# Optimization experiments

Measured on AMD Instinct MI355X. Metric: run time of the kernel, lower is better.

## Reference

```python
import jax, jax.numpy as jnp
import numpy as np

EPS = 1e-5
TAU = 2.0
HEADS = 8
SCALE = 0.125


def _bn(y, g, b, m, v):
    # y: [TB, C, N]; per-channel eval-mode batchnorm
    inv = jax.lax.rsqrt(v + EPS)
    return (y - m[:, None]) * (g * inv)[:, None] + b[:, None]


def _lif(x_seq, vth):
    # spikingjelly MultiStepLIFNode: v += (x - v)/tau, spike = H(v - vth), hard reset v*(1-s)
    def step(mem, xt):
        mem = mem + (xt - mem) / TAU
        s = (mem >= vth).astype(xt.dtype)
        mem = mem * (1.0 - s)
        return mem, s
    _, spikes = jax.lax.scan(step, jnp.zeros_like(x_seq[0]), x_seq)
    return spikes


def setup_inputs() -> dict:
    key = jax.random.key(0)
    ks = jax.random.split(key, 8)
    T, B, C, H, W = 4, 16, 256, 32, 32
    d = {
        'x': jax.random.normal(ks[0], (T, B, C, H, W), jnp.float32),
        'res_attn': jnp.zeros((1,), jnp.float32),
    }
    for i, p in enumerate(['q', 'k', 'v']):
        d[p + '_w'] = jax.random.normal(ks[1 + i], (C, C), jnp.float32) * 0.02
        d[p + '_gamma'] = jnp.ones((C,), jnp.float32)
        d[p + '_beta'] = jnp.zeros((C,), jnp.float32)
        d[p + '_mean'] = jnp.zeros((C,), jnp.float32)
        d[p + '_var'] = jnp.ones((C,), jnp.float32)
    d['p_w'] = jax.random.normal(ks[4], (C, C), jnp.float32) * 0.02
    d['p_b'] = jnp.zeros((C,), jnp.float32)
    d['p_gamma'] = jnp.ones((C,), jnp.float32)
    d['p_beta'] = jnp.zeros((C,), jnp.float32)
    d['p_mean'] = jnp.zeros((C,), jnp.float32)
    d['p_var'] = jnp.ones((C,), jnp.float32)
    return d


def reference(x, res_attn, q_w, q_gamma, q_beta, q_mean, q_var,
              k_w, k_gamma, k_beta, k_mean, k_var,
              v_w, v_gamma, v_beta, v_mean, v_var,
              p_w, p_b, p_gamma, p_beta, p_mean, p_var):
    T, B, C, H, W = x.shape
    N = H * W
    d = C // HEADS
    x2 = x.reshape(T * B, C, N)

    def branch(w, g, b, m, v):
        y = _bn(jnp.einsum('oc,bcn->bon', w, x2), g, b, m, v).reshape(T, B, C, N)
        s = _lif(y, 1.0)  # [T,B,C,N]
        # -> [T,B,heads,N,d]
        return s.transpose(0, 1, 3, 2).reshape(T, B, N, HEADS, d).transpose(0, 1, 3, 2, 4)

    q = branch(q_w, q_gamma, q_beta, q_mean, q_var)
    k = branch(k_w, k_gamma, k_beta, k_mean, k_var)
    v = branch(v_w, v_gamma, v_beta, v_mean, v_var)

    kv = jnp.einsum('tbhnd,tbhne->tbhde', k, v)      # [T,B,h,d,d]
    attn = jnp.einsum('tbhnd,tbhde->tbhne', q, kv) * SCALE  # [T,B,h,N,d]
    xa = attn.transpose(0, 1, 2, 4, 3).reshape(T, B, C, N)
    xa = _lif(xa, 0.5)

    y = _bn(jnp.einsum('oc,bcn->bon', p_w, xa.reshape(T * B, C, N)) + p_b[:, None],
            p_gamma, p_beta, p_mean, p_var)
    out = _lif(y.reshape(T, B, C, H, W), 1.0)
    return (out, v)
```

## Files before the change

### kernel.cpp

```cpp
#include <hip/hip_runtime.h>
#include <stdint.h>

typedef unsigned int u32;
typedef unsigned short ushort_t;

#define T_ 4
#define B_ 16
#define C_ 256
#define N_ 1024
#define CN (C_ * N_)
#define M_ELEMS (64 * C_ * N_)

#define OFF_S    0ull
#define OFF_YP   0ull
#define OFF_XC   67108864ull
#define OFF_SC   67108864ull
#define OFF_KV   134217728ull
#define OFF_BNS  136314880ull
#define OFF_WC   136331264ull
#define OFF_WPC  137510912ull

typedef __attribute__((ext_vector_type(8))) short bf16x8;
typedef __attribute__((ext_vector_type(4))) float f32x4;

__device__ __forceinline__ ushort_t f2bf(float f) {
  u32 u = __float_as_uint(f);
  u32 r = (u + 0x7FFFu + ((u >> 16) & 1u)) >> 16;
  return (ushort_t)r;
}
__device__ __forceinline__ float bf2f(ushort_t h) { return __uint_as_float((u32)h << 16); }

__device__ __forceinline__ void async_copy16(const void* g, void* l) {
  __builtin_amdgcn_global_load_lds(
      (const __attribute__((address_space(1))) u32*)g,
      (__attribute__((address_space(3))) u32*)l, 16, 0, 0);
}

__global__ void bn_prep(const float* __restrict__ qg, const float* __restrict__ qb2, const float* __restrict__ qm, const float* __restrict__ qv,
                        const float* __restrict__ kg, const float* __restrict__ kb, const float* __restrict__ km, const float* __restrict__ kvv,
                        const float* __restrict__ vg, const float* __restrict__ vb, const float* __restrict__ vm, const float* __restrict__ vv,
                        const float* __restrict__ pbias,
                        const float* __restrict__ pg, const float* __restrict__ pbt, const float* __restrict__ pm, const float* __restrict__ pv,
                        float* __restrict__ bns) {
  int i = threadIdx.x;
  int br = i >> 8, c = i & 255;
  const float *g, *bt, *m, *v;
  float bias = 0.f;
  if (br == 0)      { g = qg; bt = qb2; m = qm; v = qv; }
  else if (br == 1) { g = kg; bt = kb;  m = km; v = kvv; }
  else if (br == 2) { g = vg; bt = vb;  m = vm; v = vv; }
  else              { g = pg; bt = pbt; m = pm; v = pv; bias = pbias[c]; }
  float sc = g[c] / sqrtf(v[c] + 1e-5f);
  float sh = bt[c] + (bias - m[c]) * sc;
  float rcp = (sc != 0.f) ? (1.f / sc) : 0.f;
  *(float4*)&bns[4 * i] = make_float4(sc, sh, rcp, 0.f);
}

__global__ __launch_bounds__(256) void convert_w(const float* __restrict__ qw, const float* __restrict__ kw,
                                                 const float* __restrict__ vw, const float* __restrict__ pw,
                                                 ushort_t* __restrict__ Wc, ushort_t* __restrict__ Wpc) {
  int id = blockIdx.x * 256 + threadIdx.x;
  int br = id >> 16, o = (id >> 8) & 255, c = id & 255;
  const float* w = (br == 0) ? qw : (br == 1) ? kw : (br == 2) ? vw : pw;
  float f = w[o * 256 + c];
  ushort_t hi = f2bf(f);
  ushort_t lo = f2bf(f - bf2f(hi));
  if (br < 3) {
    ushort_t* d = Wc + (size_t)br * 196608 + (size_t)o * 768 + c;
    d[0] = hi; d[256] = lo; d[512] = hi;
  } else {
    ushort_t* d = Wpc + (size_t)o * 512 + c;
    d[0] = hi; d[256] = lo;
  }
}

__global__ __launch_bounds__(256) void convert_x(const float* __restrict__ x, ushort_t* __restrict__ Xc) {
  __shared__ ushort_t hi[32][260];
  __shared__ ushort_t lo[32][260];
  int bid = blockIdx.x;
  int nc = bid & 3, kb = (bid >> 2) & 7, tb = bid >> 5;
  int t = threadIdx.x;
  int n0 = nc * 256;
  const float* xb = x + (size_t)tb * CN + (size_t)(kb * 32) * N_ + n0;
#pragma unroll
  for (int p = 0; p < 8; ++p) {
    int k = p * 4 + (t >> 6);
    int n4 = (t & 63) * 4;
    float4 v = *(const float4*)&xb[(size_t)k * N_ + n4];
    ushort_t h0 = f2bf(v.x), h1 = f2bf(v.y), h2 = f2bf(v.z), h3 = f2bf(v.w);
    short4 hv = make_short4((short)h0, (short)h1, (short)h2, (short)h3);
    short4 lv = make_short4((short)f2bf(v.x - bf2f(h0)), (short)f2bf(v.y - bf2f(h1)),
                            (short)f2bf(v.z - bf2f(h2)), (short)f2bf(v.w - bf2f(h3)));
    *(short4*)&hi[k][n4] = hv;
    *(short4*)&lo[k][n4] = lv;
  }
  __syncthreads();
  ushort_t* Hs = Xc + ((size_t)(tb * 16 + kb) * 1024 + n0) * 32;
  ushort_t* Ls = Xc + ((size_t)(tb * 16 + 8 + kb) * 1024 + n0) * 32;
  int kq = t & 3;
#pragma unroll
  for (int q = 0; q < 4; ++q) {
    int n = q * 64 + (t >> 2);
    u32 a0 = (u32)hi[kq * 8 + 0][n] | ((u32)hi[kq * 8 + 1][n] << 16);
    u32 a1 = (u32)hi[kq * 8 + 2][n] | ((u32)hi[kq * 8 + 3][n] << 16);
    u32 a2 = (u32)hi[kq * 8 + 4][n] | ((u32)hi[kq * 8 + 5][n] << 16);
    u32 a3 = (u32)hi[kq * 8 + 6][n] | ((u32)hi[kq * 8 + 7][n] << 16);
    *(uint4*)(Hs + (size_t)n * 32 + kq * 8) = make_uint4(a0, a1, a2, a3);
    u32 b0 = (u32)lo[kq * 8 + 0][n] | ((u32)lo[kq * 8 + 1][n] << 16);
    u32 b1 = (u32)lo[kq * 8 + 2][n] | ((u32)lo[kq * 8 + 3][n] << 16);
    u32 b2 = (u32)lo[kq * 8 + 4][n] | ((u32)lo[kq * 8 + 5][n] << 16);
    u32 b3 = (u32)lo[kq * 8 + 6][n] | ((u32)lo[kq * 8 + 7][n] << 16);
    *(uint4*)(Ls + (size_t)n * 32 + kq * 8) = make_uint4(b0, b1, b2, b3);
  }
}

__global__ __launch_bounds__(256, 3) void gemm_qkv_lif(
    const ushort_t* __restrict__ Wc, const ushort_t* __restrict__ Xc,
    const float* __restrict__ bns, uint8_t* __restrict__ S) {
  __shared__ ushort_t Al[128 * 32];
  __shared__ ushort_t Bl[128 * 32];
  const int nt = blockIdx.x, mt = blockIdx.y, b = blockIdx.z;
  const int br = mt >> 1, rh = mt & 1;
  const ushort_t* Ab = Wc + (size_t)br * 196608 + (size_t)(rh * 128) * 768;
  const int tid = threadIdx.x;
  const int lane = tid & 63;
  const int quad = lane >> 4, r = lane & 15;
  const int w = tid >> 6;
  const int moff = (w & 1) * 64, noff = (w >> 1) * 64;
  const int c0 = tid, c1 = tid + 256;

  f32x4 acc[16];
#pragma unroll
  for (int f = 0; f < 16; ++f) acc[f] = (f32x4){0.f, 0.f, 0.f, 0.f};

  for (int t = 0; t < 4; ++t) {
    const ushort_t* Xtb = Xc + (size_t)(t * 16 + b) * 16 * 32768 + (size_t)(nt * 128) * 32;
    for (int kb = 0; kb < 24; ++kb) {
      const int kbm = (kb < 8) ? kb : kb - 8;
      const ushort_t* Acol = Ab + kb * 32;
      async_copy16(Acol + (size_t)(c0 >> 2) * 768 + (c0 & 3) * 8, &Al[c0 * 8]);
      async_copy16(Acol + (size_t)(c1 >> 2) * 768 + (c1 & 3) * 8, &Al[c1 * 8]);
      const ushort_t* Bb = Xtb + (size_t)kbm * 32768;
      async_copy16(Bb + c0 * 8, &Bl[c0 * 8]);
      async_copy16(Bb + c1 * 8, &Bl[c1 * 8]);
      __syncthreads();
      bf16x8 a0 = *(const bf16x8*)&Al[(moff + 0 * 16 + r) * 32 + quad * 8];
      bf16x8 a1 = *(const bf16x8*)&Al[(moff + 1 * 16 + r) * 32 + quad * 8];
      bf16x8 a2 = *(const bf16x8*)&Al[(moff + 2 * 16 + r) * 32 + quad * 8];
      bf16x8 a3 = *(const bf16x8*)&Al[(moff + 3 * 16 + r) * 32 + quad * 8];
      bf16x8 b0 = *(const bf16x8*)&Bl[(noff + 0 * 16 + r) * 32 + quad * 8];
      bf16x8 b1 = *(const bf16x8*)&Bl[(noff + 1 * 16 + r) * 32 + quad * 8];
      bf16x8 b2 = *(const bf16x8*)&Bl[(noff + 2 * 16 + r) * 32 + quad * 8];
      bf16x8 b3 = *(const bf16x8*)&Bl[(noff + 3 * 16 + r) * 32 + quad * 8];
      acc[0]  = __builtin_amdgcn_mfma_f32_16x16x32_bf16(a0, b0, acc[0],  0, 0, 0);
      acc[1]  = __builtin_amdgcn_mfma_f32_16x16x32_bf16(a0, b1, acc[1],  0, 0, 0);
      acc[2]  = __builtin_amdgcn_mfma_f32_16x16x32_bf16(a0, b2, acc[2],  0, 0, 0);
      acc[3]  = __builtin_amdgcn_mfma_f32_16x16x32_bf16(a0, b3, acc[3],  0, 0, 0);
      acc[4]  = __builtin_amdgcn_mfma_f32_16x16x32_bf16(a1, b0, acc[4],  0, 0, 0);
      acc[5]  = __builtin_amdgcn_mfma_f32_16x16x32_bf16(a1, b1, acc[5],  0, 0, 0);
      acc[6]  = __builtin_amdgcn_mfma_f32_16x16x32_bf16(a1, b2, acc[6],  0, 0, 0);
      acc[7]  = __builtin_amdgcn_mfma_f32_16x16x32_bf16(a1, b3, acc[7],  0, 0, 0);
      acc[8]  = __builtin_amdgcn_mfma_f32_16x16x32_bf16(a2, b0, acc[8],  0, 0, 0);
      acc[9]  = __builtin_amdgcn_mfma_f32_16x16x32_bf16(a2, b1, acc[9],  0, 0, 0);
      acc[10] = __builtin_amdgcn_mfma_f32_16x16x32_bf16(a2, b2, acc[10], 0, 0, 0);
      acc[11] = __builtin_amdgcn_mfma_f32_16x16x32_bf16(a2, b3, acc[11], 0, 0, 0);
      acc[12] = __builtin_amdgcn_mfma_f32_16x16x32_bf16(a3, b0, acc[12], 0, 0, 0);
      acc[13] = __builtin_amdgcn_mfma_f32_16x16x32_bf16(a3, b1, acc[13], 0, 0, 0);
      acc[14] = __builtin_amdgcn_mfma_f32_16x16x32_bf16(a3, b2, acc[14], 0, 0, 0);
      acc[15] = __builtin_amdgcn_mfma_f32_16x16x32_bf16(a3, b3, acc[15], 0, 0, 0);
      __syncthreads();
    }
    uint8_t* Sb = S + (size_t)br * M_ELEMS + (size_t)(t * 16 + b) * CN;
#pragma unroll
    for (int i = 0; i < 4; ++i) {
#pragma unroll
      for (int rg = 0; rg < 4; ++rg) {
        int c = rh * 128 + moff + i * 16 + quad * 4 + rg;
        float4 bn = *(const float4*)&bns[4 * (br * 256 + c)];
        float hsc = 0.5f * bn.x;
        float hsh = 0.5f * bn.y;
        float rcp = bn.z;
        uint8_t* row = Sb + (size_t)c * N_ + nt * 128 + noff + r;
#pragma unroll
        for (int j = 0; j < 4; ++j) {
          float m = acc[i * 4 + j][rg] * hsc + hsh;
          uint8_t s = (m >= 1.0f) ? 1 : 0;
          row[j * 16] = s;
          acc[i * 4 + j][rg] = s ? 0.f : m * rcp;
        }
      }
    }
  }
}

__global__ __launch_bounds__(256) void transpose_v(const uint8_t* __restrict__ SV, float* __restrict__ vout) {
  size_t o4 = ((size_t)blockIdx.x * 256 + threadIdx.x) * 4;
  int dd = (int)(o4 & 31);
  int n = (int)((o4 >> 5) & 1023);
  int h = (int)((o4 >> 15) & 7);
  int tb = (int)(o4 >> 18);
  const uint8_t* src = SV + (size_t)tb * CN + (size_t)(h * 32 + dd) * N_ + n;
  *(float4*)(vout + o4) = make_float4((float)src[0], (float)src[(size_t)N_],
                                      (float)src[2 * (size_t)N_], (float)src[3 * (size_t)N_]);
}

__global__ __launch_bounds__(256) void kv_gram(const uint8_t* __restrict__ SK,
                                               const uint8_t* __restrict__ SV,
                                               float* __restrict__ KV) {
  __shared__ uint8_t Ks[32 * 132];
  __shared__ uint8_t Vs[32 * 132];
  const int tb = blockIdx.x >> 3, h = blockIdx.x & 7;
  const uint8_t* K = SK + (size_t)tb * CN + (size_t)h * 32 * N_;
  const uint8_t* V = SV + (size_t)tb * CN + (size_t)h * 32 * N_;
  const int tid = threadIdx.x;
  const int dd = tid >> 3, e0 = (tid & 7) * 4;
  const int lr = tid >> 3, lc = (tid & 7) * 16;
  float a0 = 0.f, a1 = 0.f, a2 = 0.f, a3 = 0.f;
  for (int n0 = 0; n0 < N_; n0 += 128) {
    uint4 kk4 = *(const uint4*)(K + (size_t)lr * N_ + n0 + lc);
    uint4 vv4 = *(const uint4*)(V + (size_t)lr * N_ + n0 + lc);
    unsigned* Kw = (unsigned*)(Ks + lr * 132 + lc);
    unsigned* Vw = (unsigned*)(Vs + lr * 132 + lc);
    Kw[0] = kk4.x; Kw[1] = kk4.y; Kw[2] = kk4.z; Kw[3] = kk4.w;
    Vw[0] = vv4.x; Vw[1] = vv4.y; Vw[2] = vv4.z; Vw[3] = vv4.w;
    __syncthreads();
    for (int n = 0; n < 128; ++n) {
      float kf = (float)Ks[dd * 132 + n];
      a0 += kf * (float)Vs[(e0 + 0) * 132 + n];
      a1 += kf * (float)Vs[(e0 + 1) * 132 + n];
      a2 += kf * (float)Vs[(e0 + 2) * 132 + n];
      a3 += kf * (float)Vs[(e0 + 3) * 132 + n];
    }
    __syncthreads();
  }
  float* o = KV + (size_t)(tb * 8 + h) * 1024 + dd * 32 + e0;
  o[0] = a0; o[1] = a1; o[2] = a2; o[3] = a3;
}

__global__ __launch_bounds__(256) void attn_lif(const uint8_t* __restrict__ SQ,
                                                const float* __restrict__ KV,
                                                ushort_t* __restrict__ Sc) {
  __shared__ float kvs[1024];
  const int bid = blockIdx.x;
  const int nb = bid & 15, h = (bid >> 4) & 7, b = bid >> 7;
  const int n0 = nb * 64;
  const int tid = threadIdx.x;
  const int nl = tid & 63, eg = tid >> 6;
  float mem[8];
#pragma unroll
  for (int j = 0; j < 8; ++j) mem[j] = 0.f;
  for (int t = 0; t < 4; ++t) {
    const float* kvp = KV + (size_t)((t * B_ + b) * 8 + h) * 1024;
    *(float4*)&kvs[tid * 4] = *(const float4*)&kvp[tid * 4];
    __syncthreads();
    const uint8_t* q = SQ + (size_t)(t * B_ + b) * CN + (size_t)h * 32 * N_ + n0 + nl;
    float val[8];
#pragma unroll
    for (int j = 0; j < 8; ++j) val[j] = 0.f;
#pragma unroll 4
    for (int dd = 0; dd < 32; ++dd) {
      float qv = (float)q[(size_t)dd * N_];
#pragma unroll
      for (int j = 0; j < 8; ++j) val[j] += qv * kvs[dd * 32 + eg * 8 + j];
    }
    ushort_t pk[8];
#pragma unroll
    for (int j = 0; j < 8; ++j) {
      float a = val[j] * 0.125f;
      mem[j] += (a - mem[j]) * 0.5f;
      int s = (mem[j] >= 0.5f);
      pk[j] = s ? (ushort_t)0x3F80 : (ushort_t)0;
      if (s) mem[j] = 0.f;
    }
    uint4 o;
    o.x = (u32)pk[0] | ((u32)pk[1] << 16);
    o.y = (u32)pk[2] | ((u32)pk[3] << 16);
    o.z = (u32)pk[4] | ((u32)pk[5] << 16);
    o.w = (u32)pk[6] | ((u32)pk[7] << 16);
    *(uint4*)(Sc + ((size_t)((t * B_ + b) * 8 + h) * 1024 + n0 + nl) * 32 + eg * 8) = o;
    __syncthreads();
  }
}

__global__ __launch_bounds__(256, 3) void gemm_p_mfma(
    const ushort_t* __restrict__ Wpc, const ushort_t* __restrict__ Sc,
    const float* __restrict__ bns, float* __restrict__ YP) {
  __shared__ ushort_t Al[128 * 32];
  __shared__ ushort_t Bl[128 * 32];
  const int nt = blockIdx.x, mt = blockIdx.y, tb = blockIdx.z;
  const ushort_t* Ab = Wpc + (size_t)(mt * 128) * 512;
  const int tid = threadIdx.x;
  const int lane = tid & 63;
  const int quad = lane >> 4, r = lane & 15;
  const int w = tid >> 6;
  const int moff = (w & 1) * 64, noff = (w >> 1) * 64;
  const int c0 = tid, c1 = tid + 256;
  f32x4 acc[16];
#pragma unroll
  for (int f = 0; f < 16; ++f) acc[f] = (f32x4){0.f, 0.f, 0.f, 0.f};
  const ushort_t* Stb = Sc + (size_t)tb * 8 * 32768 + (size_t)(nt * 128) * 32;
  for (int kb = 0; kb < 16; ++kb) {
    const int kbm = (kb < 8) ? kb : kb - 8;
    const ushort_t* Acol = Ab + kb * 32;
    async_copy16(Acol + (size_t)(c0 >> 2) * 512 + (c0 & 3) * 8, &Al[c0 * 8]);
    async_copy16(Acol + (size_t)(c1 >> 2) * 512 + (c1 & 3) * 8, &Al[c1 * 8]);
    const ushort_t* Bb = Stb + (size_t)kbm * 32768;
    async_copy16(Bb + c0 * 8, &Bl[c0 * 8]);
    async_copy16(Bb + c1 * 8, &Bl[c1 * 8]);
    __syncthreads();
    bf16x8 a0 = *(const bf16x8*)&Al[(moff + 0 * 16 + r) * 32 + quad * 8];
    bf16x8 a1 = *(const bf16x8*)&Al[(moff + 1 * 16 + r) * 32 + quad * 8];
    bf16x8 a2 = *(const bf16x8*)&Al[(moff + 2 * 16 + r) * 32 + quad * 8];
    bf16x8 a3 = *(const bf16x8*)&Al[(moff + 3 * 16 + r) * 32 + quad * 8];
    bf16x8 b0 = *(const bf16x8*)&Bl[(noff + 0 * 16 + r) * 32 + quad * 8];
    bf16x8 b1 = *(const bf16x8*)&Bl[(noff + 1 * 16 + r) * 32 + quad * 8];
    bf16x8 b2 = *(const bf16x8*)&Bl[(noff + 2 * 16 + r) * 32 + quad * 8];
    bf16x8 b3 = *(const bf16x8*)&Bl[(noff + 3 * 16 + r) * 32 + quad * 8];
    acc[0]  = __builtin_amdgcn_mfma_f32_16x16x32_bf16(a0, b0, acc[0],  0, 0, 0);
    acc[1]  = __builtin_amdgcn_mfma_f32_16x16x32_bf16(a0, b1, acc[1],  0, 0, 0);
    acc[2]  = __builtin_amdgcn_mfma_f32_16x16x32_bf16(a0, b2, acc[2],  0, 0, 0);
    acc[3]  = __builtin_amdgcn_mfma_f32_16x16x32_bf16(a0, b3, acc[3],  0, 0, 0);
    acc[4]  = __builtin_amdgcn_mfma_f32_16x16x32_bf16(a1, b0, acc[4],  0, 0, 0);
    acc[5]  = __builtin_amdgcn_mfma_f32_16x16x32_bf16(a1, b1, acc[5],  0, 0, 0);
    acc[6]  = __builtin_amdgcn_mfma_f32_16x16x32_bf16(a1, b2, acc[6],  0, 0, 0);
    acc[7]  = __builtin_amdgcn_mfma_f32_16x16x32_bf16(a1, b3, acc[7],  0, 0, 0);
    acc[8]  = __builtin_amdgcn_mfma_f32_16x16x32_bf16(a2, b0, acc[8],  0, 0, 0);
    acc[9]  = __builtin_amdgcn_mfma_f32_16x16x32_bf16(a2, b1, acc[9],  0, 0, 0);
    acc[10] = __builtin_amdgcn_mfma_f32_16x16x32_bf16(a2, b2, acc[10], 0, 0, 0);
    acc[11] = __builtin_amdgcn_mfma_f32_16x16x32_bf16(a2, b3, acc[11], 0, 0, 0);
    acc[12] = __builtin_amdgcn_mfma_f32_16x16x32_bf16(a3, b0, acc[12], 0, 0, 0);
    acc[13] = __builtin_amdgcn_mfma_f32_16x16x32_bf16(a3, b1, acc[13], 0, 0, 0);
    acc[14] = __builtin_amdgcn_mfma_f32_16x16x32_bf16(a3, b2, acc[14], 0, 0, 0);
    acc[15] = __builtin_amdgcn_mfma_f32_16x16x32_bf16(a3, b3, acc[15], 0, 0, 0);
    __syncthreads();
  }
  float* Yb = YP + (size_t)tb * CN;
#pragma unroll
  for (int i = 0; i < 4; ++i) {
#pragma unroll
    for (int rg = 0; rg < 4; ++rg) {
      int c = mt * 128 + moff + i * 16 + quad * 4 + rg;
      float4 bn = *(const float4*)&bns[4 * (768 + c)];
      float sc = bn.x;
      float sh = bn.y;
      float* row = Yb + (size_t)c * N_ + nt * 128 + noff + r;
#pragma unroll
      for (int j = 0; j < 4; ++j) row[j * 16] = acc[i * 4 + j][rg] * sc + sh;
    }
  }
}

__global__ __launch_bounds__(256) void lif_out(const float* __restrict__ YP, float* __restrict__ out) {
  size_t e4 = ((size_t)blockIdx.x * 256 + threadIdx.x) * 4;
  float m0 = 0.f, m1 = 0.f, m2 = 0.f, m3 = 0.f;
#pragma unroll
  for (int t = 0; t < 4; ++t) {
    float4 y = *(const float4*)(YP + (size_t)t * (B_ * CN) + e4);
    m0 += (y.x - m0) * 0.5f;
    m1 += (y.y - m1) * 0.5f;
    m2 += (y.z - m2) * 0.5f;
    m3 += (y.w - m3) * 0.5f;
    float s0 = (m0 >= 1.0f) ? 1.f : 0.f;
    float s1 = (m1 >= 1.0f) ? 1.f : 0.f;
    float s2 = (m2 >= 1.0f) ? 1.f : 0.f;
    float s3 = (m3 >= 1.0f) ? 1.f : 0.f;
    *(float4*)(out + (size_t)t * (B_ * CN) + e4) = make_float4(s0, s1, s2, s3);
    m0 *= (1.f - s0);
    m1 *= (1.f - s1);
    m2 *= (1.f - s2);
    m3 *= (1.f - s3);
  }
}

extern "C" void kernel_launch(void* const* d_in, const int* in_sizes, int n_in,
                              void* d_out, int out_size, void* d_ws, size_t ws_size,
                              hipStream_t stream) {
  const float* x   = (const float*)d_in[0];
  const float* qw  = (const float*)d_in[2];
  const float* qg  = (const float*)d_in[3];
  const float* qb  = (const float*)d_in[4];
  const float* qm  = (const float*)d_in[5];
  const float* qv  = (const float*)d_in[6];
  const float* kw  = (const float*)d_in[7];
  const float* kg  = (const float*)d_in[8];
  const float* kb  = (const float*)d_in[9];
  const float* km  = (const float*)d_in[10];
  const float* kvv = (const float*)d_in[11];
  const float* vw  = (const float*)d_in[12];
  const float* vg  = (const float*)d_in[13];
  const float* vb  = (const float*)d_in[14];
  const float* vm  = (const float*)d_in[15];
  const float* vv  = (const float*)d_in[16];
  const float* pw  = (const float*)d_in[17];
  const float* pb  = (const float*)d_in[18];
  const float* pg  = (const float*)d_in[19];
  const float* pbt = (const float*)d_in[20];
  const float* pm  = (const float*)d_in[21];
  const float* pv  = (const float*)d_in[22];

  float* out = (float*)d_out;
  float* vout = out + M_ELEMS;

  uint8_t* ws = (uint8_t*)d_ws;
  uint8_t* S   = ws + OFF_S;
  float* YP    = (float*)(ws + OFF_YP);
  ushort_t* Xc = (ushort_t*)(ws + OFF_XC);
  ushort_t* Sc = (ushort_t*)(ws + OFF_SC);
  float* KV    = (float*)(ws + OFF_KV);
  float* BNS   = (float*)(ws + OFF_BNS);
  ushort_t* Wc  = (ushort_t*)(ws + OFF_WC);
  ushort_t* Wpc = (ushort_t*)(ws + OFF_WPC);

  bn_prep<<<dim3(1), dim3(1024), 0, stream>>>(qg, qb, qm, qv, kg, kb, km, kvv,
                                              vg, vb, vm, vv, pb, pg, pbt, pm, pv, BNS);
  convert_w<<<dim3(1024), dim3(256), 0, stream>>>(qw, kw, vw, pw, Wc, Wpc);
  convert_x<<<dim3(2048), dim3(256), 0, stream>>>(x, Xc);
  gemm_qkv_lif<<<dim3(8, 6, 16), dim3(256), 0, stream>>>(Wc, Xc, BNS, S);
  transpose_v<<<dim3(16384), dim3(256), 0, stream>>>(S + 2ull * M_ELEMS, vout);
  kv_gram<<<dim3(512), dim3(256), 0, stream>>>(S + 1ull * M_ELEMS, S + 2ull * M_ELEMS, KV);
  attn_lif<<<dim3(2048), dim3(256), 0, stream>>>(S, KV, Sc);
  gemm_p_mfma<<<dim3(8, 2, 64), dim3(256), 0, stream>>>(Wpc, Sc, BNS, YP);
  lif_out<<<dim3(4096), dim3(256), 0, stream>>>(YP, out);
}
```

Measured before the change: 446.8 us.

## Widen GEMM K-steps to 64 and reuse shared B tiles across hi/lo weight halves

Restructures the QKV and projection GEMM main loops to process two 32-wide K slices per barrier pair instead of one. Each loaded B tile (activation hi part) is reused for both the hi and lo split-bf16 weight halves, cutting redundant global-to-LDS loads of B and halving the number of barriers. In the QKV kernel the lo activation tiles are loaded in a second phase into a reused buffer. LDS use per block triples (48KB), which may lower occupancy below the launch-bounds target of 3 blocks per CU.

```diff
diff --git a/kernel.cpp b/kernel.cpp
--- a/kernel.cpp
+++ b/kernel.cpp
@@ -34,6 +34,31 @@
   __builtin_amdgcn_global_load_lds(
       (const __attribute__((address_space(1))) u32*)g,
       (__attribute__((address_space(3))) u32*)l, 16, 0, 0);
+}
+
+__device__ __forceinline__ void mfma_grp(const ushort_t* Ap, int aoff,
+                                         bf16x8 b0, bf16x8 b1, bf16x8 b2, bf16x8 b3,
+                                         f32x4* acc) {
+  bf16x8 a0 = *(const bf16x8*)&Ap[aoff + 0 * 16 * 32];
+  bf16x8 a1 = *(const bf16x8*)&Ap[aoff + 1 * 16 * 32];
+  bf16x8 a2 = *(const bf16x8*)&Ap[aoff + 2 * 16 * 32];
+  bf16x8 a3 = *(const bf16x8*)&Ap[aoff + 3 * 16 * 32];
+  acc[0]  = __builtin_amdgcn_mfma_f32_16x16x32_bf16(a0, b0, acc[0],  0, 0, 0);
+  acc[1]  = __builtin_amdgcn_mfma_f32_16x16x32_bf16(a0, b1, acc[1],  0, 0, 0);
+  acc[2]  = __builtin_amdgcn_mfma_f32_16x16x32_bf16(a0, b2, acc[2],  0, 0, 0);
+  acc[3]  = __builtin_amdgcn_mfma_f32_16x16x32_bf16(a0, b3, acc[3],  0, 0, 0);
+  acc[4]  = __builtin_amdgcn_mfma_f32_16x16x32_bf16(a1, b0, acc[4],  0, 0, 0);
+  acc[5]  = __builtin_amdgcn_mfma_f32_16x16x32_bf16(a1, b1, acc[5],  0, 0, 0);
+  acc[6]  = __builtin_amdgcn_mfma_f32_16x16x32_bf16(a1, b2, acc[6],  0, 0, 0);
+  acc[7]  = __builtin_amdgcn_mfma_f32_16x16x32_bf16(a1, b3, acc[7],  0, 0, 0);
+  acc[8]  = __builtin_amdgcn_mfma_f32_16x16x32_bf16(a2, b0, acc[8],  0, 0, 0);
+  acc[9]  = __builtin_amdgcn_mfma_f32_16x16x32_bf16(a2, b1, acc[9],  0, 0, 0);
+  acc[10] = __builtin_amdgcn_mfma_f32_16x16x32_bf16(a2, b2, acc[10], 0, 0, 0);
+  acc[11] = __builtin_amdgcn_mfma_f32_16x16x32_bf16(a2, b3, acc[11], 0, 0, 0);
+  acc[12] = __builtin_amdgcn_mfma_f32_16x16x32_bf16(a3, b0, acc[12], 0, 0, 0);
+  acc[13] = __builtin_amdgcn_mfma_f32_16x16x32_bf16(a3, b1, acc[13], 0, 0, 0);
+  acc[14] = __builtin_amdgcn_mfma_f32_16x16x32_bf16(a3, b2, acc[14], 0, 0, 0);
+  acc[15] = __builtin_amdgcn_mfma_f32_16x16x32_bf16(a3, b3, acc[15], 0, 0, 0);
 }
 
 __global__ void bn_prep(const float* __restrict__ qg, const float* __restrict__ qb2, const float* __restrict__ qm, const float* __restrict__ qv,
@@ -117,8 +142,9 @@
 __global__ __launch_bounds__(256, 3) void gemm_qkv_lif(
     const ushort_t* __restrict__ Wc, const ushort_t* __restrict__ Xc,
     const float* __restrict__ bns, uint8_t* __restrict__ S) {
-  __shared__ ushort_t Al[128 * 32];
-  __shared__ ushort_t Bl[128 * 32];
+  __shared__ ushort_t Ah[2][4096];
+  __shared__ ushort_t Xl[2][4096];
+  __shared__ ushort_t Bh[2][4096];
   const int nt = blockIdx.x, mt = blockIdx.y, b = blockIdx.z;
   const int br = mt >> 1, rh = mt & 1;
   const ushort_t* Ab = Wc + (size_t)br * 196608 + (size_t)(rh * 128) * 768;
@@ -128,6 +154,8 @@
   const int w = tid >> 6;
   const int moff = (w & 1) * 64, noff = (w >> 1) * 64;
   const int c0 = tid, c1 = tid + 256;
+  const int aoff = (moff + r) * 32 + quad * 8;
+  const int boff = (noff + r) * 32 + quad * 8;
 
   f32x4 acc[16];
 #pragma unroll
@@ -135,39 +163,62 @@
 
   for (int t = 0; t < 4; ++t) {
     const ushort_t* Xtb = Xc + (size_t)(t * 16 + b) * 16 * 32768 + (size_t)(nt * 128) * 32;
-    for (int kb = 0; kb < 24; ++kb) {
-      const int kbm = (kb < 8) ? kb : kb - 8;
-      const ushort_t* Acol = Ab + kb * 32;
-      async_copy16(Acol + (size_t)(c0 >> 2) * 768 + (c0 & 3) * 8, &Al[c0 * 8]);
-      async_copy16(Acol + (size_t)(c1 >> 2) * 768 + (c1 & 3) * 8, &Al[c1 * 8]);
-      const ushort_t* Bb = Xtb + (size_t)kbm * 32768;
-      async_copy16(Bb + c0 * 8, &Bl[c0 * 8]);
-      async_copy16(Bb + c1 * 8, &Bl[c1 * 8]);
+    for (int p = 0; p < 4; ++p) {
+      const ushort_t* AcH = Ab + p * 64;
+      const ushort_t* AcL = Ab + 256 + p * 64;
+      const ushort_t* Bh0 = Xtb + (size_t)(2 * p) * 32768;
+      const ushort_t* Bh1 = Bh0 + 32768;
+      async_copy16(AcH + (size_t)(c0 >> 2) * 768 + (c0 & 3) * 8,      &Ah[0][c0 * 8]);
+      async_copy16(AcH + (size_t)(c1 >> 2) * 768 + (c1 & 3) * 8,      &Ah[0][c1 * 8]);
+      async_copy16(AcH + (size_t)(c0 >> 2) * 768 + 32 + (c0 & 3) * 8, &Ah[1][c0 * 8]);
+      async_copy16(AcH + (size_t)(c1 >> 2) * 768 + 32 + (c1 & 3) * 8, &Ah[1][c1 * 8]);
+      async_copy16(AcL + (size_t)(c0 >> 2) * 768 + (c0 & 3) * 8,      &Xl[0][c0 * 8]);
+      async_copy16(AcL + (size_t)(c1 >> 2) * 768 + (c1 & 3) * 8,      &Xl[0][c1 * 8]);
+      async_copy16(AcL + (size_t)(c0 >> 2) * 768 + 32 + (c0 & 3) * 8, &Xl[1][c0 * 8]);
+      async_copy16(AcL + (size_t)(c1 >> 2) * 768 + 32 + (c1 & 3) * 8, &Xl[1][c1 * 8]);
+      async_copy16(Bh0 + c0 * 8, &Bh[0][c0 * 8]);
+      async_copy16(Bh0 + c1 * 8, &Bh[0][c1 * 8]);
+      async_copy16(Bh1 + c0 * 8, &Bh[1][c0 * 8]);
+      async_copy16(Bh1 + c1 * 8, &Bh[1][c1 * 8]);
       __syncthreads();
-      bf16x8 a0 = *(const bf16x8*)&Al[(moff + 0 * 16 + r) * 32 + quad * 8];
-      bf16x8 a1 = *(const bf16x8*)&Al[(moff + 1 * 16 + r) * 32 + quad * 8];
-      bf16x8 a2 = *(const bf16x8*)&Al[(moff + 2 * 16 + r) * 32 + quad * 8];
-      bf16x8 a3 = *(const bf16x8*)&Al[(moff + 3 * 16 + r) * 32 + quad * 8];
-      bf16x8 b0 = *(const bf16x8*)&Bl[(noff + 0 * 16 + r) * 32 + quad * 8];
-      bf16x8 b1 = *(const bf16x8*)&Bl[(noff + 1 * 16 + r) * 32 + quad * 8];
-      bf16x8 b2 = *(const bf16x8*)&Bl[(noff + 2 * 16 + r) * 32 + quad * 8];
-      bf16x8 b3 = *(const bf16x8*)&Bl[(noff + 3 * 16 + r) * 32 + quad * 8];
-      acc[0]  = __builtin_amdgcn_mfma_f32_16x16x32_bf16(a0, b0, acc[0],  0, 0, 0);
-      acc[1]  = __builtin_amdgcn_mfma_f32_16x16x32_bf16(a0, b1, acc[1],  0, 0, 0);
-      acc[2]  = __builtin_amdgcn_mfma_f32_16x16x32_bf16(a0, b2, acc[2],  0, 0, 0);
-      acc[3]  = __builtin_amdgcn_mfma_f32_16x16x32_bf16(a0, b3, acc[3],  0, 0, 0);
-      acc[4]  = __builtin_amdgcn_mfma_f32_16x16x32_bf16(a1, b0, acc[4],  0, 0, 0);
-      acc[5]  = __builtin_amdgcn_mfma_f32_16x16x32_bf16(a1, b1, acc[5],  0, 0, 0);
-      acc[6]  = __builtin_amdgcn_mfma_f32_16x16x32_bf16(a1, b2, acc[6],  0, 0, 0);
-      acc[7]  = __builtin_amdgcn_mfma_f32_16x16x32_bf16(a1, b3, acc[7],  0, 0, 0);
-      acc[8]  = __builtin_amdgcn_mfma_f32_16x16x32_bf16(a2, b0, acc[8],  0, 0, 0);
-      acc[9]  = __builtin_amdgcn_mfma_f32_16x16x32_bf16(a2, b1, acc[9],  0, 0, 0);
-      acc[10] = __builtin_amdgcn_mfma_f32_16x16x32_bf16(a2, b2, acc[10], 0, 0, 0);
-      acc[11] = __builtin_amdgcn_mfma_f32_16x16x32_bf16(a2, b3, acc[11], 0, 0, 0);
-      acc[12] = __builtin_amdgcn_mfma_f32_16x16x32_bf16(a3, b0, acc[12], 0, 0, 0);
-      acc[13] = __builtin_amdgcn_mfma_f32_16x16x32_bf16(a3, b1, acc[13], 0, 0, 0);
-      acc[14] = __builtin_amdgcn_mfma_f32_16x16x32_bf16(a3, b2, acc[14], 0, 0, 0);
-      acc[15] = __builtin_amdgcn_mfma_f32_16x16x32_bf16(a3, b3, acc[15], 0, 0, 0);
+      {
+        bf16x8 b0 = *(const bf16x8*)&Bh[0][boff + 0 * 16 * 32];
+        bf16x8 b1 = *(const bf16x8*)&Bh[0][boff + 1 * 16 * 32];
+        bf16x8 b2 = *(const bf16x8*)&Bh[0][boff + 2 * 16 * 32];
+        bf16x8 b3 = *(const bf16x8*)&Bh[0][boff + 3 * 16 * 32];
+        mfma_grp(&Ah[0][0], aoff, b0, b1, b2, b3, acc);
+        mfma_grp(&Xl[0][0], aoff, b0, b1, b2, b3, acc);
+      }
+      {
+        bf16x8 b0 = *(const bf16x8*)&Bh[1][boff + 0 * 16 * 32];
+        bf16x8 b1 = *(const bf16x8*)&Bh[1][boff + 1 * 16 * 32];
+        bf16x8 b2 = *(const bf16x8*)&Bh[1][boff + 2 * 16 * 32];
+        bf16x8 b3 = *(const bf16x8*)&Bh[1][boff + 3 * 16 * 32];
+        mfma_grp(&Ah[1][0], aoff, b0, b1, b2, b3, acc);
+        mfma_grp(&Xl[1][0], aoff, b0, b1, b2, b3, acc);
+      }
+      __syncthreads();
+      const ushort_t* Bl0 = Xtb + (size_t)(8 + 2 * p) * 32768;
+      const ushort_t* Bl1 = Bl0 + 32768;
+      async_copy16(Bl0 + c0 * 8, &Xl[0][c0 * 8]);
+      async_copy16(Bl0 + c1 * 8, &Xl[0][c1 * 8]);
+      async_copy16(Bl1 + c0 * 8, &Xl[1][c0 * 8]);
+      async_copy16(Bl1 + c1 * 8, &Xl[1][c1 * 8]);
+      __syncthreads();
+      {
+        bf16x8 b0 = *(const bf16x8*)&Xl[0][boff + 0 * 16 * 32];
+        bf16x8 b1 = *(const bf16x8*)&Xl[0][boff + 1 * 16 * 32];
+        bf16x8 b2 = *(const bf16x8*)&Xl[0][boff + 2 * 16 * 32];
+        bf16x8 b3 = *(const bf16x8*)&Xl[0][boff + 3 * 16 * 32];
+        mfma_grp(&Ah[0][0], aoff, b0, b1, b2, b3, acc);
+      }
+      {
+        bf16x8 b0 = *(const bf16x8*)&Xl[1][boff + 0 * 16 * 32];
+        bf16x8 b1 = *(const bf16x8*)&Xl[1][boff + 1 * 16 * 32];
+        bf16x8 b2 = *(const bf16x8*)&Xl[1][boff + 2 * 16 * 32];
+        bf16x8 b3 = *(const bf16x8*)&Xl[1][boff + 3 * 16 * 32];
+        mfma_grp(&Ah[1][0], aoff, b0, b1, b2, b3, acc);
+      }
       __syncthreads();
     }
     uint8_t* Sb = S + (size_t)br * M_ELEMS + (size_t)(t * 16 + b) * CN;
@@ -285,8 +336,9 @@
 __global__ __launch_bounds__(256, 3) void gemm_p_mfma(
     const ushort_t* __restrict__ Wpc, const ushort_t* __restrict__ Sc,
     const float* __restrict__ bns, float* __restrict__ YP) {
-  __shared__ ushort_t Al[128 * 32];
-  __shared__ ushort_t Bl[128 * 32];
+  __shared__ ushort_t Ah[2][4096];
+  __shared__ ushort_t Al[2][4096];
+  __shared__ ushort_t Bs[2][4096];
   const int nt = blockIdx.x, mt = blockIdx.y, tb = blockIdx.z;
   const ushort_t* Ab = Wpc + (size_t)(mt * 128) * 512;
   const int tid = threadIdx.x;
@@ -295,43 +347,46 @@
   const int w = tid >> 6;
   const int moff = (w & 1) * 64, noff = (w >> 1) * 64;
   const int c0 = tid, c1 = tid + 256;
+  const int aoff = (moff + r) * 32 + quad * 8;
+  const int boff = (noff + r) * 32 + quad * 8;
   f32x4 acc[16];
 #pragma unroll
   for (int f = 0; f < 16; ++f) acc[f] = (f32x4){0.f, 0.f, 0.f, 0.f};
   const ushort_t* Stb = Sc + (size_t)tb * 8 * 32768 + (size_t)(nt * 128) * 32;
-  for (int kb = 0; kb < 16; ++kb) {
-    const int kbm = (kb < 8) ? kb : kb - 8;
-    const ushort_t* Acol = Ab + kb * 32;
-    async_copy16(Acol + (size_t)(c0 >> 2) * 512 + (c0 & 3) * 8, &Al[c0 * 8]);
-    async_copy16(Acol + (size_t)(c1 >> 2) * 512 + (c1 & 3) * 8, &Al[c1 * 8]);
-    const ushort_t* Bb = Stb + (size_t)kbm * 32768;
-    async_copy16(Bb + c0 * 8, &Bl[c0 * 8]);
-    async_copy16(Bb + c1 * 8, &Bl[c1 * 8]);
-    __syncthreads();
-    bf16x8 a0 = *(const bf16x8*)&Al[(moff + 0 * 16 + r) * 32 + quad * 8];
-    bf16x8 a1 = *(const bf16x8*)&Al[(moff + 1 * 16 + r) * 32 + quad * 8];
-    bf16x8 a2 = *(const bf16x8*)&Al[(moff + 2 * 16 + r) * 32 + quad * 8];
-    bf16x8 a3 = *(const bf16x8*)&Al[(moff + 3 * 16 + r) * 32 + quad * 8];
-    bf16x8 b0 = *(const bf16x8*)&Bl[(noff + 0 * 16 + r) * 32 + quad * 8];
-    bf16x8 b1 = *(const bf16x8*)&Bl[(noff + 1 * 16 + r) * 32 + quad * 8];
-    bf16x8 b2 = *(const bf16x8*)&Bl[(noff + 2 * 16 + r) * 32 + quad * 8];
-    bf16x8 b3 = *(const bf16x8*)&Bl[(noff + 3 * 16 + r) * 32 + quad * 8];
-    acc[0]  = __builtin_amdgcn_mfma_f32_16x16x32_bf16(a0, b0, acc[0],  0, 0, 0);
-    acc[1]  = __builtin_amdgcn_mfma_f32_16x16x32_bf16(a0, b1, acc[1],  0, 0, 0);
-    acc[2]  = __builtin_amdgcn_mfma_f32_16x16x32_bf16(a0, b2, acc[2],  0, 0, 0);
-    acc[3]  = __builtin_amdgcn_mfma_f32_16x16x32_bf16(a0, b3, acc[3],  0, 0, 0);
-    acc[4]  = __builtin_amdgcn_mfma_f32_16x16x32_bf16(a1, b0, acc[4],  0, 0, 0);
-    acc[5]  = __builtin_amdgcn_mfma_f32_16x16x32_bf16(a1, b1, acc[5],  0, 0, 0);
-    acc[6]  = __builtin_amdgcn_mfma_f32_16x16x32_bf16(a1, b2, acc[6],  0, 0, 0);
-    acc[7]  = __builtin_amdgcn_mfma_f32_16x16x32_bf16(a1, b3, acc[7],  0, 0, 0);
-    acc[8]  = __builtin_amdgcn_mfma_f32_16x16x32_bf16(a2, b0, acc[8],  0, 0, 0);
-    acc[9]  = __builtin_amdgcn_mfma_f32_16x16x32_bf16(a2, b1, acc[9],  0, 0, 0);
-    acc[10] = __builtin_amdgcn_mfma_f32_16x16x32_bf16(a2, b2, acc[10], 0, 0, 0);
-    acc[11] = __builtin_amdgcn_mfma_f32_16x16x32_bf16(a2, b3, acc[11], 0, 0, 0);
-    acc[12] = __builtin_amdgcn_mfma_f32_16x16x32_bf16(a3, b0, acc[12], 0, 0, 0);
-    acc[13] = __builtin_amdgcn_mfma_f32_16x16x32_bf16(a3, b1, acc[13], 0, 0, 0);
-    acc[14] = __builtin_amdgcn_mfma_f32_16x16x32_bf16(a3, b2, acc[14], 0, 0, 0);
-    acc[15] = __builtin_amdgcn_mfma_f32_16x16x32_bf16(a3, b3, acc[15], 0, 0, 0);
+  for (int p = 0; p < 4; ++p) {
+    const ushort_t* AcH = Ab + p * 64;
+    const ushort_t* AcL = Ab + 256 + p * 64;
+    const ushort_t* Bb0 = Stb + (size_t)(2 * p) * 32768;
+    const ushort_t* Bb1 = Bb0 + 32768;
+    async_copy16(AcH + (size_t)(c0 >> 2) * 512 + (c0 & 3) * 8,      &Ah[0][c0 * 8]);
+    async_copy16(AcH + (size_t)(c1 >> 2) * 512 + (c1 & 3) * 8,      &Ah[0][c1 * 8]);
+    async_copy16(AcH + (size_t)(c0 >> 2) * 512 + 32 + (c0 & 3) * 8, &Ah[1][c0 * 8]);
+    async_copy16(AcH + (size_t)(c1 >> 2) * 512 + 32 + (c1 & 3) * 8, &Ah[1][c1 * 8]);
+    async_copy16(AcL + (size_t)(c0 >> 2) * 512 + (c0 & 3) * 8,      &Al[0][c0 * 8]);
+    async_copy16(AcL + (size_t)(c1 >> 2) * 512 + (c1 & 3) * 8,      &Al[0][c1 * 8]);
+    async_copy16(AcL + (size_t)(c0 >> 2) * 512 + 32 + (c0 & 3) * 8, &Al[1][c0 * 8]);
+    async_copy16(AcL + (size_t)(c1 >> 2) * 512 + 32 + (c1 & 3) * 8, &Al[1][c1 * 8]);
+    async_copy16(Bb0 + c0 * 8, &Bs[0][c0 * 8]);
+    async_copy16(Bb0 + c1 * 8, &Bs[0][c1 * 8]);
+    async_copy16(Bb1 + c0 * 8, &Bs[1][c0 * 8]);
+    async_copy16(Bb1 + c1 * 8, &Bs[1][c1 * 8]);
+    __syncthreads();
+    {
+      bf16x8 b0 = *(const bf16x8*)&Bs[0][boff + 0 * 16 * 32];
+      bf16x8 b1 = *(const bf16x8*)&Bs[0][boff + 1 * 16 * 32];
+      bf16x8 b2 = *(const bf16x8*)&Bs[0][boff + 2 * 16 * 32];
+      bf16x8 b3 = *(const bf16x8*)&Bs[0][boff + 3 * 16 * 32];
+      mfma_grp(&Ah[0][0], aoff, b0, b1, b2, b3, acc);
+      mfma_grp(&Al[0][0], aoff, b0, b1, b2, b3, acc);
+    }
+    {
+      bf16x8 b0 = *(const bf16x8*)&Bs[1][boff + 0 * 16 * 32];
+      bf16x8 b1 = *(const bf16x8*)&Bs[1][boff + 1 * 16 * 32];
+      bf16x8 b2 = *(const bf16x8*)&Bs[1][boff + 2 * 16 * 32];
+      bf16x8 b3 = *(const bf16x8*)&Bs[1][boff + 3 * 16 * 32];
+      mfma_grp(&Ah[1][0], aoff, b0, b1, b2, b3, acc);
+      mfma_grp(&Al[1][0], aoff, b0, b1, b2, b3, acc);
+    }
     __syncthreads();
   }
   float* Yb = YP + (size_t)tb * CN;
```

Result: faster. 433.9 us (-2.9%).
